# Optimization experiments

Hardware: AMD Instinct MI355X
Metric: run time of the kernel (lower is better)

## Reference

```python
import jax, jax.numpy as jnp
import numpy as np

B, F, D, V = 8192, 26, 32, 100000
H1, H2 = 128, 128  # cin_size
U1, U2 = 400, 400  # dnn hidden units


def setup_inputs() -> dict:
    key = jax.random.key(0)
    ks = jax.random.split(key, 12)
    s = 0.05  # keep activations/sigmoid in a sane range
    return {
        "dense_inputs": jax.random.normal(ks[0], (B, 13), jnp.float32),
        "sparse_inputs": jax.random.randint(ks[1], (B, F), 0, V, jnp.int32),
        "E": jax.random.normal(ks[2], (F, V, D), jnp.float32) * s,
        "W_cin0": jax.random.normal(ks[3], (F, F, H1), jnp.float32) * s,
        "W_cin1": jax.random.normal(ks[4], (F, H1, H2), jnp.float32) * s,
        "W1": jax.random.normal(ks[5], (F * D, U1), jnp.float32) * s,
        "b1": jnp.zeros((U1,), jnp.float32),
        "W2": jax.random.normal(ks[6], (U1, U2), jnp.float32) * s,
        "b2": jnp.zeros((U2,), jnp.float32),
        "w_lin": jax.random.normal(ks[7], (F, 1), jnp.float32) * s,
        "b_lin": jnp.zeros((1,), jnp.float32),
        "w_out": jax.random.normal(ks[8], (1 + H1 + H2 + U2 + 13, 1), jnp.float32) * s,
        "b_out": jnp.zeros((1,), jnp.float32),
    }


def reference(dense_inputs, sparse_inputs, E, W_cin0, W_cin1, W1, b1, W2, b2,
              w_lin, b_lin, w_out, b_out):
    # Linear part: Dense(1) applied to raw (cast) sparse ids, as in the TF code.
    linear_out = sparse_inputs.astype(jnp.float32) @ w_lin + b_lin  # [B,1]

    # Embedding lookup: per-field tables. embed[b,f,:] = E[f, sparse[b,f], :]
    embed = E[jnp.arange(F)[None, :], sparse_inputs]  # [B,F,D]

    # CIN. The split->matmul->reshape->conv1d chain is exactly:
    #   x_{k+1}[b,h,d] = sum_{i,j} W_k[i,j,h] * X0[b,i,d] * x_k[b,j,d]
    X0 = embed
    x1 = jnp.einsum('bid,bjd,ijh->bhd', X0, X0, W_cin0)   # [B,H1,D]
    x2 = jnp.einsum('bid,bjd,ijh->bhd', X0, x1, W_cin1)   # [B,H2,D]
    cin_out = jnp.concatenate([x1, x2], axis=1).sum(axis=-1)  # [B,H1+H2]

    # DNN on flattened embeddings (dropout rate 0 -> identity at inference).
    v = embed.reshape(B, F * D)
    h = jax.nn.relu(v @ W1 + b1)
    h = jax.nn.relu(h @ W2 + b2)  # [B,U2]

    total = jnp.concatenate([linear_out, cin_out, h, dense_inputs], axis=-1)
    return jax.nn.sigmoid(total @ w_out + b_out)  # [B,1]
```

## Files before the change

### kernel.cpp

```cpp
#include <hip/hip_runtime.h>
#include <hip/hip_bf16.h>
#include <math.h>

typedef __attribute__((ext_vector_type(8))) short bf16x8;
typedef __attribute__((ext_vector_type(4))) float f32x4;

#define B_ 8192
#define F_ 26
#define D_ 32
#define V_ 100000
#define NP_ 351
#define KP_ 352

static const size_t OFF_VB    = 0;
static const size_t OFF_LIN   = 13631488;
static const size_t OFF_CIN1  = 13664256;
static const size_t OFF_CIN2P = 17858560;
static const size_t OFF_G     = 26247168;
static const size_t OFF_H1B   = 80773120;
static const size_t OFF_H2    = 87326720;
static const size_t OFF_W0T   = 100433920;
static const size_t OFF_WC1T  = 100524032;
static const size_t OFF_W1T   = 101376000;
static const size_t OFF_W2T   = 102041600;

static __device__ __forceinline__ unsigned short f2b(float f) {
    unsigned int u = __float_as_uint(f);
    unsigned int r = (u + 0x7FFF + ((u >> 16) & 1)) >> 16;
    return (unsigned short)r;
}
static __device__ __forceinline__ unsigned int pk2(float a, float b) {
    return (unsigned int)f2b(a) | ((unsigned int)f2b(b) << 16);
}
static __device__ __forceinline__ float bf2f(unsigned short u) {
    return __uint_as_float(((unsigned int)u) << 16);
}

__global__ __launch_bounds__(256) void k0a_w0(const float* __restrict__ W0,
                                              unsigned short* __restrict__ W0t) {
    int g = blockIdx.x * 256 + threadIdx.x;
    if (g >= 128 * KP_) return;
    int h = g / KP_, p = g % KP_;
    float w = 0.f;
    if (p < NP_) {
        int i = 0, base = 0;
        while (base + (F_ - i) <= p) { base += F_ - i; ++i; }
        int j = i + (p - base);
        w = W0[(i * F_ + j) * 128 + h];
        if (i != j) w += W0[(j * F_ + i) * 128 + h];
    }
    W0t[g] = f2b(w);
}

__global__ __launch_bounds__(256) void tkern(const float* __restrict__ src,
                                             unsigned short* __restrict__ dst,
                                             int K, int N) {
    __shared__ float tl[32][33];
    const int lx = threadIdx.x & 31, ly = threadIdx.x >> 5;
    const int n0 = blockIdx.x * 32, k0 = blockIdx.y * 32;
#pragma unroll
    for (int i = 0; i < 4; ++i) {
        int k = k0 + ly + i * 8, n = n0 + lx;
        if (k < K && n < N) tl[ly + i * 8][lx] = src[(size_t)k * N + n];
    }
    __syncthreads();
#pragma unroll
    for (int i = 0; i < 4; ++i) {
        int n = n0 + ly + i * 8, k = k0 + lx;
        if (k < K && n < N) dst[(size_t)n * K + k] = f2b(tl[lx][ly + i * 8]);
    }
}

__global__ __launch_bounds__(256) void k1_embed_cin(
    const int*   __restrict__ sparse,
    const float* __restrict__ E,
    const unsigned short* __restrict__ W0t,
    const float* __restrict__ wlin,
    const float* __restrict__ blin,
    unsigned short* __restrict__ vb,
    float* __restrict__ lin,
    float* __restrict__ cin1,
    unsigned short* __restrict__ G)
{
    __shared__ __align__(16) unsigned short embB[32][40];
    __shared__ __align__(16) unsigned short P[32][360];
    __shared__ __align__(16) unsigned short x1s[128][40];
    __shared__ float cin1t[2][128];
    __shared__ float linb[F_];
    __shared__ int   idxs[F_];
    __shared__ unsigned char pI[KP_], pJ[KP_];

    const int b = blockIdx.x, t = threadIdx.x;

    if (t < F_) {
        int id = sparse[b * F_ + t];
        idxs[t] = id;
        linb[t] = (float)id * wlin[t];
        int i = t, base = F_ * i - (i * (i - 1)) / 2;
        for (int j = i; j < F_; ++j) { pI[base + j - i] = (unsigned char)i; pJ[base + j - i] = (unsigned char)j; }
    }
    __syncthreads();

    if (t < 208) {
        int f = t >> 3, q = t & 7;
        float4 r = *(const float4*)(E + ((size_t)f * V_ + idxs[f]) * D_ + q * 4);
        ushort4 u;
        u.x = f2b(r.x); u.y = f2b(r.y); u.z = f2b(r.z); u.w = f2b(r.w);
        *(ushort4*)&embB[f][q * 4] = u;
        *(ushort4*)(vb + (size_t)b * 832 + f * 32 + q * 4) = u;
    }
    if (t >= 208 && t < 208 + 96) {
        int o = t - 208;
        *(unsigned int*)&embB[26 + (o >> 4)][(o & 15) * 2] = 0u;
    }
    __syncthreads();

    {
        const int d = t & 31, pb = t >> 5;
        const int p0 = pb * 44;
        for (int k = 0; k < 22; ++k) {
            int p = p0 + 2 * k;
            float a  = bf2f(embB[pI[p]][d]) * bf2f(embB[pJ[p]][d]);
            float c2 = (p + 1 < NP_) ? bf2f(embB[pI[p + 1]][d]) * bf2f(embB[pJ[p + 1]][d]) : 0.f;
            *(unsigned int*)&P[d][p] = pk2(a, c2);
        }
        if (t == 0) { float s = blin[0]; for (int f = 0; f < F_; ++f) s += linb[f]; lin[b] = s; }
    }
    __syncthreads();

    const int wave = t >> 6, lane = t & 63;
    const int lr = lane & 15, lg = lane >> 4;
    const int mt = wave & 1, ntb = (wave >> 1) * 4;
    f32x4 acc[4] = {};
    {
        const unsigned short* Arow = &P[mt * 16 + lr][lg * 8];
        for (int kt = 0; kt < 11; ++kt) {
            bf16x8 af = *(const bf16x8*)(Arow + kt * 32);
#pragma unroll
            for (int n = 0; n < 4; ++n) {
                const unsigned short* bp = W0t + (size_t)((ntb + n) * 16 + lr) * KP_ + kt * 32 + lg * 8;
                bf16x8 bfg = *(const bf16x8*)bp;
                acc[n] = __builtin_amdgcn_mfma_f32_16x16x32_bf16(af, bfg, acc[n], 0, 0, 0);
            }
        }
    }
#pragma unroll
    for (int n = 0; n < 4; ++n) {
        float s = acc[n][0] + acc[n][1] + acc[n][2] + acc[n][3];
        s += __shfl_xor(s, 16, 64);
        s += __shfl_xor(s, 32, 64);
        int h = (ntb + n) * 16 + lr;
        if (lg == 0) cin1t[mt][h] = s;
        int d0 = mt * 16 + lg * 4;
        *(unsigned int*)&x1s[h][d0]     = pk2(acc[n][0], acc[n][1]);
        *(unsigned int*)&x1s[h][d0 + 2] = pk2(acc[n][2], acc[n][3]);
    }
    __syncthreads();

    if (t < 128) cin1[(size_t)b * 128 + t] = cin1t[0][t] + cin1t[1][t];

    {
        bf16x8 ea = *(const bf16x8*)&embB[mt * 16 + lr][lg * 8];
#pragma unroll
        for (int n = 0; n < 4; ++n) {
            bf16x8 xb = *(const bf16x8*)&x1s[(ntb + n) * 16 + lr][lg * 8];
            f32x4 g = {};
            g = __builtin_amdgcn_mfma_f32_16x16x32_bf16(ea, xb, g, 0, 0, 0);
            int j = (ntb + n) * 16 + lr;
            int i0 = mt * 16 + lg * 4;
#pragma unroll
            for (int r = 0; r < 4; ++r) {
                int i = i0 + r;
                if (i < F_) G[(size_t)b * 3328 + i * 128 + j] = f2b(g[r]);
            }
        }
    }
}

template<bool RELU, bool BIAS, bool OUTB, bool SPLIT>
__global__ __launch_bounds__(256) void gemm2(
    const unsigned short* __restrict__ A,
    const unsigned short* __restrict__ Bt,
    const float* __restrict__ bias,
    void* __restrict__ C,
    int M, int N, int K, int lda, int ldb, int kchunk)
{
    __shared__ __align__(16) unsigned short As[64][40];
    __shared__ __align__(16) unsigned short Bs[128][40];
    const int t = threadIdx.x;
    const int m0 = blockIdx.y * 64, n0 = blockIdx.x * 128;
    const int z = SPLIT ? blockIdx.z : 0;
    const int kbase = z * kchunk;
    const int Keff = min(kchunk, K - kbase);
    const int wave = t >> 6, lane = t & 63;
    const int lr = lane & 15, lg = lane >> 4;
    const int wn = wave * 32;
    const int ar = t >> 2, kg = (t & 3) * 8;

    const unsigned short* aptr  = A  + (size_t)(m0 + ar) * lda + kbase + kg;
    const unsigned short* bptr0 = Bt + (size_t)(n0 + ar) * ldb + kbase + kg;
    const unsigned short* bptr1 = Bt + (size_t)(n0 + 64 + ar) * ldb + kbase + kg;
    const bool bn0 = (n0 + ar) < N, bn1 = (n0 + 64 + ar) < N;

    const uint4 z4 = make_uint4(0u, 0u, 0u, 0u);
    uint4 av, bv0, bv1;
    av  = (kg < Keff)        ? *(const uint4*)(aptr)  : z4;
    bv0 = (bn0 && kg < Keff) ? *(const uint4*)(bptr0) : z4;
    bv1 = (bn1 && kg < Keff) ? *(const uint4*)(bptr1) : z4;

    f32x4 acc[4][2] = {};
    const int nkt = (Keff + 31) >> 5;
    for (int kt = 0; kt < nkt; ++kt) {
        *(uint4*)&As[ar][kg]      = av;
        *(uint4*)&Bs[ar][kg]      = bv0;
        *(uint4*)&Bs[64 + ar][kg] = bv1;
        __syncthreads();
        int kn = (kt + 1) * 32 + kg;
        if (kt + 1 < nkt) {
            av  = (kn < Keff)        ? *(const uint4*)(aptr  + (kt + 1) * 32) : z4;
            bv0 = (bn0 && kn < Keff) ? *(const uint4*)(bptr0 + (kt + 1) * 32) : z4;
            bv1 = (bn1 && kn < Keff) ? *(const uint4*)(bptr1 + (kt + 1) * 32) : z4;
        }
        bf16x8 af[4], bfr[2];
#pragma unroll
        for (int i = 0; i < 4; ++i) af[i]  = *(const bf16x8*)&As[i * 16 + lr][lg * 8];
#pragma unroll
        for (int j = 0; j < 2; ++j) bfr[j] = *(const bf16x8*)&Bs[wn + j * 16 + lr][lg * 8];
#pragma unroll
        for (int i = 0; i < 4; ++i)
#pragma unroll
            for (int j = 0; j < 2; ++j)
                acc[i][j] = __builtin_amdgcn_mfma_f32_16x16x32_bf16(af[i], bfr[j], acc[i][j], 0, 0, 0);
        __syncthreads();
    }

#pragma unroll
    for (int i = 0; i < 4; ++i) {
        int mrow = m0 + i * 16 + lg * 4;
#pragma unroll
        for (int j = 0; j < 2; ++j) {
            int col = n0 + wn + j * 16 + lr;
            if (col >= N) continue;
            float bb = BIAS ? bias[col] : 0.f;
#pragma unroll
            for (int r = 0; r < 4; ++r) {
                float vv = acc[i][j][r] + bb;
                if (RELU) vv = fmaxf(vv, 0.f);
                if (OUTB) ((unsigned short*)C)[(size_t)(mrow + r) * N + col] = f2b(vv);
                else      ((float*)C)[(SPLIT ? (size_t)z * M * N : (size_t)0) + (size_t)(mrow + r) * N + col] = vv;
            }
        }
    }
}

__global__ __launch_bounds__(256) void k3_final(
    const float* __restrict__ lin,
    const float* __restrict__ cin1,
    const float* __restrict__ cin2p,
    const float* __restrict__ h2,
    const float* __restrict__ dense,
    const float* __restrict__ wout,
    const float* __restrict__ bout,
    float* __restrict__ out)
{
    const int wave = threadIdx.x >> 6, lane = threadIdx.x & 63;
    const int b = blockIdx.x * 4 + wave;
    float s = 0.f;
    for (int o = lane; o < 670; o += 64) {
        float f;
        if (o == 0)        f = lin[b];
        else if (o < 129)  f = cin1[(size_t)b * 128 + (o - 1)];
        else if (o < 257) {
            size_t idx = (size_t)b * 128 + (o - 129);
            f = cin2p[idx] + cin2p[(size_t)B_ * 128 + idx];
        }
        else if (o < 657)  f = h2[(size_t)b * 400 + (o - 257)];
        else               f = dense[(size_t)b * 13 + (o - 657)];
        s = fmaf(f, wout[o], s);
    }
#pragma unroll
    for (int off = 32; off > 0; off >>= 1) s += __shfl_down(s, off, 64);
    if (lane == 0) out[b] = 1.f / (1.f + expf(-(s + bout[0])));
}

extern "C" void kernel_launch(void* const* d_in, const int* in_sizes, int n_in,
                              void* d_out, int out_size, void* d_ws, size_t ws_size,
                              hipStream_t stream) {
    const float* dense  = (const float*)d_in[0];
    const int*   sparse = (const int*)  d_in[1];
    const float* E      = (const float*)d_in[2];
    const float* W0     = (const float*)d_in[3];
    const float* Wc1    = (const float*)d_in[4];
    const float* W1     = (const float*)d_in[5];
    const float* b1     = (const float*)d_in[6];
    const float* W2     = (const float*)d_in[7];
    const float* b2     = (const float*)d_in[8];
    const float* wlin   = (const float*)d_in[9];
    const float* blin   = (const float*)d_in[10];
    const float* wout   = (const float*)d_in[11];
    const float* bout   = (const float*)d_in[12];
    float* out = (float*)d_out;

    char* ws = (char*)d_ws;
    unsigned short* vb    = (unsigned short*)(ws + OFF_VB);
    float*          lin   = (float*)(ws + OFF_LIN);
    float*          cin1  = (float*)(ws + OFF_CIN1);
    float*          cin2p = (float*)(ws + OFF_CIN2P);
    unsigned short* G     = (unsigned short*)(ws + OFF_G);
    unsigned short* h1b   = (unsigned short*)(ws + OFF_H1B);
    float*          h2    = (float*)(ws + OFF_H2);
    unsigned short* W0t   = (unsigned short*)(ws + OFF_W0T);
    unsigned short* Wc1t  = (unsigned short*)(ws + OFF_WC1T);
    unsigned short* W1t   = (unsigned short*)(ws + OFF_W1T);
    unsigned short* W2t   = (unsigned short*)(ws + OFF_W2T);

    k0a_w0<<<(128 * KP_ + 255) / 256, 256, 0, stream>>>(W0, W0t);
    tkern<<<dim3(4, 104), 256, 0, stream>>>(Wc1, Wc1t, 3328, 128);
    tkern<<<dim3(13, 26), 256, 0, stream>>>(W1, W1t, 832, 400);
    tkern<<<dim3(13, 13), 256, 0, stream>>>(W2, W2t, 400, 400);

    k1_embed_cin<<<B_, 256, 0, stream>>>(sparse, E, W0t, wlin, blin, vb, lin, cin1, G);

    gemm2<false, false, false, true ><<<dim3(1, 128, 2), 256, 0, stream>>>(G,   Wc1t, nullptr, cin2p, B_, 128, 3328, 3328, 3328, 1664);
    gemm2<true,  true,  true,  false><<<dim3(4, 128, 1), 256, 0, stream>>>(vb,  W1t,  b1,      h1b,   B_, 400, 832,  832,  832,  832);
    gemm2<true,  true,  false, false><<<dim3(4, 128, 1), 256, 0, stream>>>(h1b, W2t,  b2,      h2,    B_, 400, 400,  400,  400,  400);

    k3_final<<<B_ / 4, 256, 0, stream>>>(lin, cin1, cin2p, h2, dense, wout, bout, out);
}
```

Baseline: 582.4 us.

## Merge weight prep and independent GEMMs into fewer launches, use truncating bf16 packs

Folds the four weight-preparation kernels into one launch and runs the h1 GEMM and the CIN layer-2 GEMM as one grid, with the CIN GEMM split four ways along K so both halves have 512 blocks each. The final kernel now sums four partial buffers. Bf16 conversion of embeddings, products and outputs switches from round-to-nearest to truncation via a byte-permute pack, which lowers ALU work but adds rounding bias. This cuts launch overhead and raises occupancy for the split-K CIN GEMM, at the cost of extra partial-sum traffic.

```diff
diff --git a/kernel.cpp b/kernel.cpp
--- a/kernel.cpp
+++ b/kernel.cpp
@@ -16,48 +16,35 @@
 static const size_t OFF_LIN   = 13631488;
 static const size_t OFF_CIN1  = 13664256;
 static const size_t OFF_CIN2P = 17858560;
-static const size_t OFF_G     = 26247168;
-static const size_t OFF_H1B   = 80773120;
-static const size_t OFF_H2    = 87326720;
-static const size_t OFF_W0T   = 100433920;
-static const size_t OFF_WC1T  = 100524032;
-static const size_t OFF_W1T   = 101376000;
-static const size_t OFF_W2T   = 102041600;
+static const size_t OFF_G     = 34635776;
+static const size_t OFF_H1B   = 89161728;
+static const size_t OFF_H2    = 95715328;
+static const size_t OFF_W0T   = 108822528;
+static const size_t OFF_WC1T  = 108912640;
+static const size_t OFF_W1T   = 109764608;
+static const size_t OFF_W2T   = 110430208;
 
 static __device__ __forceinline__ unsigned short f2b(float f) {
     unsigned int u = __float_as_uint(f);
-    unsigned int r = (u + 0x7FFF + ((u >> 16) & 1)) >> 16;
-    return (unsigned short)r;
-}
-static __device__ __forceinline__ unsigned int pk2(float a, float b) {
-    return (unsigned int)f2b(a) | ((unsigned int)f2b(b) << 16);
+    return (unsigned short)((u + 0x7FFF + ((u >> 16) & 1)) >> 16);
+}
+static __device__ __forceinline__ unsigned short f2bt(float f) {
+    return (unsigned short)(__float_as_uint(f) >> 16);
+}
+static __device__ __forceinline__ unsigned int pk2t(float a, float b) {
+    return __builtin_amdgcn_perm(__float_as_uint(b), __float_as_uint(a), 0x07060302u);
 }
 static __device__ __forceinline__ float bf2f(unsigned short u) {
     return __uint_as_float(((unsigned int)u) << 16);
 }
 
-__global__ __launch_bounds__(256) void k0a_w0(const float* __restrict__ W0,
-                                              unsigned short* __restrict__ W0t) {
-    int g = blockIdx.x * 256 + threadIdx.x;
-    if (g >= 128 * KP_) return;
-    int h = g / KP_, p = g % KP_;
-    float w = 0.f;
-    if (p < NP_) {
-        int i = 0, base = 0;
-        while (base + (F_ - i) <= p) { base += F_ - i; ++i; }
-        int j = i + (p - base);
-        w = W0[(i * F_ + j) * 128 + h];
-        if (i != j) w += W0[(j * F_ + i) * 128 + h];
-    }
-    W0t[g] = f2b(w);
-}
-
-__global__ __launch_bounds__(256) void tkern(const float* __restrict__ src,
-                                             unsigned short* __restrict__ dst,
-                                             int K, int N) {
+static __device__ __forceinline__ void transpose_body(
+    const float* __restrict__ src, unsigned short* __restrict__ dst,
+    int K, int N, int bx, int by)
+{
     __shared__ float tl[32][33];
     const int lx = threadIdx.x & 31, ly = threadIdx.x >> 5;
-    const int n0 = blockIdx.x * 32, k0 = blockIdx.y * 32;
+    const int n0 = bx * 32, k0 = by * 32;
 #pragma unroll
     for (int i = 0; i < 4; ++i) {
         int k = k0 + ly + i * 8, n = n0 + lx;
@@ -69,6 +56,37 @@
         int n = n0 + ly + i * 8, k = k0 + lx;
         if (k < K && n < N) dst[(size_t)n * K + k] = f2b(tl[lx][ly + i * 8]);
     }
+}
+
+__global__ __launch_bounds__(256) void k0_all(
+    const float* __restrict__ W0, const float* __restrict__ Wc1,
+    const float* __restrict__ W1, const float* __restrict__ W2,
+    unsigned short* __restrict__ W0t, unsigned short* __restrict__ Wc1t,
+    unsigned short* __restrict__ W1t, unsigned short* __restrict__ W2t)
+{
+    int bid = blockIdx.x;
+    if (bid < 176) {
+        int g = bid * 256 + threadIdx.x;
+        if (g < 128 * KP_) {
+            int h = g / KP_, p = g % KP_;
+            float w = 0.f;
+            if (p < NP_) {
+                int i = 0, base = 0;
+                while (base + (F_ - i) <= p) { base += F_ - i; ++i; }
+                int j = i + (p - base);
+                w = W0[(i * F_ + j) * 128 + h];
+                if (i != j) w += W0[(j * F_ + i) * 128 + h];
+            }
+            W0t[g] = f2b(w);
+        }
+        return;
+    }
+    bid -= 176;
+    const float* src; unsigned short* dst; int K, N, nx;
+    if (bid < 416)               { src = Wc1; dst = Wc1t; K = 3328; N = 128; nx = 4; }
+    else if ((bid -= 416) < 338) { src = W1;  dst = W1t;  K = 832;  N = 400; nx = 13; }
+    else                         { bid -= 338; src = W2; dst = W2t; K = 400; N = 400; nx = 13; }
+    transpose_body(src, dst, K, N, bid % nx, bid / nx);
 }
 
 __global__ __launch_bounds__(256) void k1_embed_cin(
@@ -104,10 +122,11 @@
     if (t < 208) {
         int f = t >> 3, q = t & 7;
         float4 r = *(const float4*)(E + ((size_t)f * V_ + idxs[f]) * D_ + q * 4);
-        ushort4 u;
-        u.x = f2b(r.x); u.y = f2b(r.y); u.z = f2b(r.z); u.w = f2b(r.w);
-        *(ushort4*)&embB[f][q * 4] = u;
-        *(ushort4*)(vb + (size_t)b * 832 + f * 32 + q * 4) = u;
+        uint2 uu;
+        uu.x = pk2t(r.x, r.y);
+        uu.y = pk2t(r.z, r.w);
+        *(uint2*)&embB[f][q * 4] = uu;
+        *(uint2*)(vb + (size_t)b * 832 + f * 32 + q * 4) = uu;
     }
     if (t >= 208 && t < 208 + 96) {
         int o = t - 208;
@@ -122,7 +141,7 @@
             int p = p0 + 2 * k;
             float a  = bf2f(embB[pI[p]][d]) * bf2f(embB[pJ[p]][d]);
             float c2 = (p + 1 < NP_) ? bf2f(embB[pI[p + 1]][d]) * bf2f(embB[pJ[p + 1]][d]) : 0.f;
-            *(unsigned int*)&P[d][p] = pk2(a, c2);
+            *(unsigned int*)&P[d][p] = pk2t(a, c2);
         }
         if (t == 0) { float s = blin[0]; for (int f = 0; f < F_; ++f) s += linb[f]; lin[b] = s; }
     }
@@ -152,8 +171,8 @@
         int h = (ntb + n) * 16 + lr;
         if (lg == 0) cin1t[mt][h] = s;
         int d0 = mt * 16 + lg * 4;
-        *(unsigned int*)&x1s[h][d0]     = pk2(acc[n][0], acc[n][1]);
-        *(unsigned int*)&x1s[h][d0 + 2] = pk2(acc[n][2], acc[n][3]);
+        *(unsigned int*)&x1s[h][d0]     = pk2t(acc[n][0], acc[n][1]);
+        *(unsigned int*)&x1s[h][d0 + 2] = pk2t(acc[n][2], acc[n][3]);
     }
     __syncthreads();
 
@@ -171,45 +190,122 @@
 #pragma unroll
             for (int r = 0; r < 4; ++r) {
                 int i = i0 + r;
-                if (i < F_) G[(size_t)b * 3328 + i * 128 + j] = f2b(g[r]);
+                if (i < F_) G[(size_t)b * 3328 + i * 128 + j] = f2bt(g[r]);
             }
         }
     }
 }
 
-template<bool RELU, bool BIAS, bool OUTB, bool SPLIT>
-__global__ __launch_bounds__(256) void gemm2(
-    const unsigned short* __restrict__ A,
-    const unsigned short* __restrict__ Bt,
-    const float* __restrict__ bias,
-    void* __restrict__ C,
-    int M, int N, int K, int lda, int ldb, int kchunk)
+static __device__ __forceinline__ void gemm_body(
+    const unsigned short* __restrict__ A, int lda, int kbase,
+    const unsigned short* __restrict__ Bt, int ldb, int N,
+    const float* __restrict__ bias, bool relu, bool outb,
+    void* __restrict__ C, int ldc, int m0, int n0,
+    unsigned short (*As)[40], unsigned short (*Bs)[40])
+{
+    const int t = threadIdx.x;
+    const int wave = t >> 6, lane = t & 63;
+    const int lr = lane & 15, lg = lane >> 4;
+    const int wn = wave * 32;
+    const int ar = t >> 2, kg = (t & 3) * 8;
+
+    const unsigned short* aptr = A  + (size_t)(m0 + ar) * lda + kbase + kg;
+    const unsigned short* bp0  = Bt + (size_t)(n0 + ar) * ldb + kbase + kg;
+    const unsigned short* bp1  = Bt + (size_t)(n0 + 64 + ar) * ldb + kbase + kg;
+    const bool bn0 = (n0 + ar) < N, bn1 = (n0 + 64 + ar) < N;
+
+    const uint4 z4 = make_uint4(0u, 0u, 0u, 0u);
+    uint4 av  = *(const uint4*)aptr;
+    uint4 bv0 = bn0 ? *(const uint4*)bp0 : z4;
+    uint4 bv1 = bn1 ? *(const uint4*)bp1 : z4;
+
+    f32x4 acc[4][2] = {};
+    for (int kt = 0; kt < 26; ++kt) {
+        *(uint4*)&As[ar][kg]      = av;
+        *(uint4*)&Bs[ar][kg]      = bv0;
+        *(uint4*)&Bs[64 + ar][kg] = bv1;
+        __syncthreads();
+        if (kt + 1 < 26) {
+            av  = *(const uint4*)(aptr + (kt + 1) * 32);
+            bv0 = bn0 ? *(const uint4*)(bp0 + (kt + 1) * 32) : z4;
+            bv1 = bn1 ? *(const uint4*)(bp1 + (kt + 1) * 32) : z4;
+        }
+        bf16x8 af[4], bfr[2];
+#pragma unroll
+        for (int i = 0; i < 4; ++i) af[i]  = *(const bf16x8*)&As[i * 16 + lr][lg * 8];
+#pragma unroll
+        for (int j = 0; j < 2; ++j) bfr[j] = *(const bf16x8*)&Bs[wn + j * 16 + lr][lg * 8];
+#pragma unroll
+        for (int i = 0; i < 4; ++i)
+#pragma unroll
+            for (int j = 0; j < 2; ++j)
+                acc[i][j] = __builtin_amdgcn_mfma_f32_16x16x32_bf16(af[i], bfr[j], acc[i][j], 0, 0, 0);
+        __syncthreads();
+    }
+#pragma unroll
+    for (int i = 0; i < 4; ++i) {
+        int mrow = m0 + i * 16 + lg * 4;
+#pragma unroll
+        for (int j = 0; j < 2; ++j) {
+            int col = n0 + wn + j * 16 + lr;
+            if (col >= N) continue;
+            float bb = bias ? bias[col] : 0.f;
+#pragma unroll
+            for (int r = 0; r < 4; ++r) {
+                float vv = acc[i][j][r] + bb;
+                if (relu) vv = fmaxf(vv, 0.f);
+                if (outb) ((unsigned short*)C)[(size_t)(mrow + r) * ldc + col] = f2bt(vv);
+                else      ((float*)C)[(size_t)(mrow + r) * ldc + col] = vv;
+            }
+        }
+    }
+}
+
+__global__ __launch_bounds__(256) void k2_h1_cin2(
+    const unsigned short* __restrict__ vb, const unsigned short* __restrict__ W1t,
+    const float* __restrict__ b1, unsigned short* __restrict__ h1b,
+    const unsigned short* __restrict__ G, const unsigned short* __restrict__ Wc1t,
+    float* __restrict__ cin2p)
+{
+    __shared__ __align__(16) unsigned short As[64][40];
+    __shared__ __align__(16) unsigned short Bs[128][40];
+    const int m0 = blockIdx.y * 64;
+    if (blockIdx.z == 0) {
+        gemm_body(vb, 832, 0, W1t, 832, 400, b1, true, true, h1b, 400,
+                  m0, blockIdx.x * 128, As, Bs);
+    } else {
+        float* Cp = cin2p + (size_t)blockIdx.x * B_ * 128;
+        gemm_body(G, 3328, blockIdx.x * 832, Wc1t, 3328, 128, nullptr, false, false, Cp, 128,
+                  m0, 0, As, Bs);
+    }
+}
+
+__global__ __launch_bounds__(256) void k2_h2(
+    const unsigned short* __restrict__ A, const unsigned short* __restrict__ Bt,
+    const float* __restrict__ bias, float* __restrict__ C)
 {
     __shared__ __align__(16) unsigned short As[64][40];
     __shared__ __align__(16) unsigned short Bs[128][40];
     const int t = threadIdx.x;
     const int m0 = blockIdx.y * 64, n0 = blockIdx.x * 128;
-    const int z = SPLIT ? blockIdx.z : 0;
-    const int kbase = z * kchunk;
-    const int Keff = min(kchunk, K - kbase);
+    const int N = 400, K = 400, ld = 400;
     const int wave = t >> 6, lane = t & 63;
     const int lr = lane & 15, lg = lane >> 4;
     const int wn = wave * 32;
     const int ar = t >> 2, kg = (t & 3) * 8;
 
-    const unsigned short* aptr  = A  + (size_t)(m0 + ar) * lda + kbase + kg;
-    const unsigned short* bptr0 = Bt + (size_t)(n0 + ar) * ldb + kbase + kg;
-    const unsigned short* bptr1 = Bt + (size_t)(n0 + 64 + ar) * ldb + kbase + kg;
+    const unsigned short* aptr = A  + (size_t)(m0 + ar) * ld + kg;
+    const unsigned short* bp0  = Bt + (size_t)(n0 + ar) * ld + kg;
+    const unsigned short* bp1  = Bt + (size_t)(n0 + 64 + ar) * ld + kg;
     const bool bn0 = (n0 + ar) < N, bn1 = (n0 + 64 + ar) < N;
-
     const uint4 z4 = make_uint4(0u, 0u, 0u, 0u);
     uint4 av, bv0, bv1;
-    av  = (kg < Keff)        ? *(const uint4*)(aptr)  : z4;
-    bv0 = (bn0 && kg < Keff) ? *(const uint4*)(bptr0) : z4;
-    bv1 = (bn1 && kg < Keff) ? *(const uint4*)(bptr1) : z4;
+    av  = (kg < K)        ? *(const uint4*)aptr : z4;
+    bv0 = (bn0 && kg < K) ? *(const uint4*)bp0  : z4;
+    bv1 = (bn1 && kg < K) ? *(const uint4*)bp1  : z4;
 
     f32x4 acc[4][2] = {};
-    const int nkt = (Keff + 31) >> 5;
+    const int nkt = 13;
     for (int kt = 0; kt < nkt; ++kt) {
         *(uint4*)&As[ar][kg]      = av;
         *(uint4*)&Bs[ar][kg]      = bv0;
@@ -217,9 +313,9 @@
         __syncthreads();
         int kn = (kt + 1) * 32 + kg;
         if (kt + 1 < nkt) {
-            av  = (kn < Keff)        ? *(const uint4*)(aptr  + (kt + 1) * 32) : z4;
-            bv0 = (bn0 && kn < Keff) ? *(const uint4*)(bptr0 + (kt + 1) * 32) : z4;
-            bv1 = (bn1 && kn < Keff) ? *(const uint4*)(bptr1 + (kt + 1) * 32) : z4;
+            av  = (kn < K)        ? *(const uint4*)(aptr + (kt + 1) * 32) : z4;
+            bv0 = (bn0 && kn < K) ? *(const uint4*)(bp0  + (kt + 1) * 32) : z4;
+            bv1 = (bn1 && kn < K) ? *(const uint4*)(bp1  + (kt + 1) * 32) : z4;
         }
         bf16x8 af[4], bfr[2];
 #pragma unroll
@@ -233,7 +329,6 @@
                 acc[i][j] = __builtin_amdgcn_mfma_f32_16x16x32_bf16(af[i], bfr[j], acc[i][j], 0, 0, 0);
         __syncthreads();
     }
-
 #pragma unroll
     for (int i = 0; i < 4; ++i) {
         int mrow = m0 + i * 16 + lg * 4;
@@ -241,14 +336,10 @@
         for (int j = 0; j < 2; ++j) {
             int col = n0 + wn + j * 16 + lr;
             if (col >= N) continue;
-            float bb = BIAS ? bias[col] : 0.f;
-#pragma unroll
-            for (int r = 0; r < 4; ++r) {
-                float vv = acc[i][j][r] + bb;
-                if (RELU) vv = fmaxf(vv, 0.f);
-                if (OUTB) ((unsigned short*)C)[(size_t)(mrow + r) * N + col] = f2b(vv);
-                else      ((float*)C)[(SPLIT ? (size_t)z * M * N : (size_t)0) + (size_t)(mrow + r) * N + col] = vv;
-            }
+            float bb = bias[col];
+#pragma unroll
+            for (int r = 0; r < 4; ++r)
+                C[(size_t)(mrow + r) * N + col] = fmaxf(acc[i][j][r] + bb, 0.f);
         }
     }
 }
@@ -265,6 +356,7 @@
 {
     const int wave = threadIdx.x >> 6, lane = threadIdx.x & 63;
     const int b = blockIdx.x * 4 + wave;
+    const size_t S = (size_t)B_ * 128;
     float s = 0.f;
     for (int o = lane; o < 670; o += 64) {
         float f;
@@ -272,7 +364,7 @@
         else if (o < 129)  f = cin1[(size_t)b * 128 + (o - 1)];
         else if (o < 257) {
             size_t idx = (size_t)b * 128 + (o - 129);
-            f = cin2p[idx] + cin2p[(size_t)B_ * 128 + idx];
+            f = (cin2p[idx] + cin2p[S + idx]) + (cin2p[2 * S + idx] + cin2p[3 * S + idx]);
         }
         else if (o < 657)  f = h2[(size_t)b * 400 + (o - 257)];
         else               f = dense[(size_t)b * 13 + (o - 657)];
@@ -314,16 +406,9 @@
     unsigned short* W1t   = (unsigned short*)(ws + OFF_W1T);
     unsigned short* W2t   = (unsigned short*)(ws + OFF_W2T);
 
-    k0a_w0<<<(128 * KP_ + 255) / 256, 256, 0, stream>>>(W0, W0t);
-    tkern<<<dim3(4, 104), 256, 0, stream>>>(Wc1, Wc1t, 3328, 128);
-    tkern<<<dim3(13, 26), 256, 0, stream>>>(W1, W1t, 832, 400);
-    tkern<<<dim3(13, 13), 256, 0, stream>>>(W2, W2t, 400, 400);
-
+    k0_all<<<176 + 416 + 338 + 169, 256, 0, stream>>>(W0, Wc1, W1, W2, W0t, Wc1t, W1t, W2t);
     k1_embed_cin<<<B_, 256, 0, stream>>>(sparse, E, W0t, wlin, blin, vb, lin, cin1, G);
-
-    gemm2<false, false, false, true ><<<dim3(1, 128, 2), 256, 0, stream>>>(G,   Wc1t, nullptr, cin2p, B_, 128, 3328, 3328, 3328, 1664);
-    gemm2<true,  true,  true,  false><<<dim3(4, 128, 1), 256, 0, stream>>>(vb,  W1t,  b1,      h1b,   B_, 400, 832,  832,  832,  832);
-    gemm2<true,  true,  false, false><<<dim3(4, 128, 1), 256, 0, stream>>>(h1b, W2t,  b2,      h2,    B_, 400, 400,  400,  400,  400);
-
+    k2_h1_cin2<<<dim3(4, 128, 2), 256, 0, stream>>>(vb, W1t, b1, h1b, G, Wc1t, cin2p);
+    k2_h2<<<dim3(4, 128), 256, 0, stream>>>(h1b, W2t, b2, h2);
     k3_final<<<B_ / 4, 256, 0, stream>>>(lin, cin1, cin2p, h2, dense, wout, bout, out);
 }
```

New measurement: 561.1 us. -3.7%, faster.
